# Performance work log

Hardware: AMD Instinct MI355X
Metric: run time of the kernel (lower is better)

## Reference

```python
import jax, jax.numpy as jnp
import numpy as np

BS, L, D = 128, 256, 512
H, DK = 2, 256  # heads, head dim
EPS_BN = 1e-5


def _lin(x, W, b):
    # torch Linear: W is (out, in)
    return jnp.einsum('...i,oi->...o', x, W) + b


def _bn(x, g, b, m, v):
    # eval-mode BatchNorm over channel axis = last axis of x
    return (x - m) * (g * jax.lax.rsqrt(v + EPS_BN)) + b


def setup_inputs() -> dict:
    key = jax.random.key(0)
    ks = iter(jax.random.split(key, 64))
    rn = lambda shape, s=0.02: jax.random.normal(next(ks), shape, dtype=jnp.float32) * s
    inp = {}
    inp['cap_emb'] = jax.random.normal(next(ks), (BS, L, D), dtype=jnp.float32)
    inp['lengths'] = jax.random.randint(next(ks), (BS,), 1, L + 1, dtype=jnp.int64 if jax.config.jax_enable_x64 else jnp.int32)
    # GA linears q,k,v
    for nm in ('Wq', 'Wk', 'Wv'):
        inp[nm] = rn((D, D))
    for nm in ('bq', 'bk', 'bv'):
        inp[nm] = rn((D,))
    inp['Wfq'] = rn((DK, DK)); inp['bfq'] = rn((DK,))
    inp['Wfk'] = rn((DK, DK)); inp['bfk'] = rn((DK,))
    inp['Wfg'] = rn((2 * DK, DK)); inp['bfg'] = rn((2 * DK,))
    # BatchNorm params (eval running stats)
    for pre in ('bn1', 'bn2', 'bn3'):
        inp[pre + '_g'] = 1.0 + rn((D,), 0.1)
        inp[pre + '_b'] = rn((D,), 0.1)
        inp[pre + '_m'] = rn((D,), 0.1)
        inp[pre + '_v'] = jax.random.uniform(next(ks), (D,), minval=0.5, maxval=1.5, dtype=jnp.float32)
    # Conv1d weights, torch layout (out, in, k)
    inp['Wc2'] = rn((D, D, 2)); inp['bc2'] = rn((D,))
    inp['Wc3'] = rn((D, D, 3)); inp['bc3'] = rn((D,))
    # MLP 512 -> 1024 -> 512
    inp['Wm1'] = rn((2 * D, D)); inp['bm1'] = rn((2 * D,))
    inp['Wm2'] = rn((D, 2 * D)); inp['bm2'] = rn((D,))
    return inp


def _forward(cap_emb, Wq, bq, Wk, bk, Wv, bv, Wfq, bfq, Wfk, bfk, Wfg, bfg,
             bn1_g, bn1_b, bn1_m, bn1_v, Wc2, bc2, bn2_g, bn2_b, bn2_m, bn2_v,
             Wc3, bc3, bn3_g, bn3_b, bn3_m, bn3_v, Wm1, bm1, Wm2, bm2, lengths):
    bs, seq, dim = cap_emb.shape
    # ---- GA: gated self-attention ----
    def split_heads(x):
        return x.reshape(bs, seq, H, DK).transpose(0, 2, 1, 3)  # [bs,h,seq,dk]
    q = split_heads(_lin(cap_emb, Wq, bq))
    k = split_heads(_lin(cap_emb, Wk, bk))
    v = split_heads(_lin(cap_emb, Wv, bv))
    G = _lin(q, Wfq, bfq) * _lin(k, Wfk, bfk)
    M = jax.nn.sigmoid(_lin(G, Wfg, bfg))  # [bs,h,seq,2*dk]
    qg = q * M[..., :DK]
    kg = k * M[..., DK:]
    # torch.div(..., rounding_mode='floor') == elementwise floor of scaled scores
    scores = jnp.floor(jnp.einsum('bhqd,bhkd->bhqk', qg, kg) / jnp.sqrt(jnp.float32(DK)))
    p_attn = jax.nn.softmax(scores, axis=-1)
    x = jnp.einsum('bhqk,bhkd->bhqd', p_attn, v)
    x = x.transpose(0, 2, 1, 3).reshape(bs, seq, dim)
    # BN over features (eval), dropout is identity in eval mode
    ga_emb = cap_emb + _bn(x, bn1_g, bn1_b, bn1_m, bn1_v)
    # ---- dual conv1d branches ----
    xc = cap_emb.transpose(0, 2, 1)  # [bs, D, L]
    dn = ('NCW', 'OIW', 'NCW')
    c2 = jax.lax.conv_general_dilated(xc, Wc2, window_strides=(2,), padding='VALID', dimension_numbers=dn) + bc2[None, :, None]
    c3 = jax.lax.conv_general_dilated(xc, Wc3, window_strides=(3,), padding='VALID', dimension_numbers=dn) + bc3[None, :, None]
    f2 = jax.nn.relu(_bn(c2.transpose(0, 2, 1), bn2_g, bn2_b, bn2_m, bn2_v))
    f3 = jax.nn.relu(_bn(c3.transpose(0, 2, 1), bn3_g, bn3_b, bn3_m, bn3_v))
    ga_jw = jnp.concatenate([ga_emb, f2, f3], axis=1)
    # ---- residual MLP (dropout identity in eval) ----
    hid = jax.nn.relu(_lin(ga_jw, Wm1, bm1))
    tex_emb = _lin(hid, Wm2, bm2) + ga_jw
    # ---- length-indexed gather ----
    idx = lengths.astype(jnp.int32) - 1
    out = tex_emb[jnp.arange(bs), idx]  # [bs, D]
    # l2norm
    norm = jnp.sqrt(jnp.sum(out * out, axis=-1, keepdims=True)) + 1e-8
    return out / norm


def reference(cap_emb, lengths, Wq, bq, Wk, bk, Wv, bv, Wfq, bfq, Wfk, bfk, Wfg, bfg,
              bn1_g, bn1_b, bn1_m, bn1_v, Wc2, bc2, bn2_g, bn2_b, bn2_m, bn2_v,
              Wc3, bc3, bn3_g, bn3_b, bn3_m, bn3_v, Wm1, bm1, Wm2, bm2):
    return _forward(cap_emb, Wq, bq, Wk, bk, Wv, bv, Wfq, bfq, Wfk, bfk, Wfg, bfg,
                    bn1_g, bn1_b, bn1_m, bn1_v, Wc2, bc2, bn2_g, bn2_b, bn2_m, bn2_v,
                    Wc3, bc3, bn3_g, bn3_b, bn3_m, bn3_v, Wm1, bm1, Wm2, bm2, lengths)
```

## Files before the change

kernel.cpp:

```cpp
#include <hip/hip_runtime.h>
#include <math.h>


typedef short bf16x8 __attribute__((ext_vector_type(8)));
typedef float f32x4 __attribute__((ext_vector_type(4)));
typedef short short4v __attribute__((ext_vector_type(4)));

__device__ __forceinline__ short f2bf(float x) {
    union { float f; unsigned u; } c; c.f = x;
    unsigned r = c.u + 0x7FFFu + ((c.u >> 16) & 1u);
    return (short)(r >> 16);
}
__device__ __forceinline__ float bf2f(short h) {
    union { float f; unsigned u; } c; c.u = ((unsigned)(unsigned short)h) << 16;
    return c.f;
}
__device__ __forceinline__ void glds16(const void* g, void* l) {
    __builtin_amdgcn_global_load_lds(
        (const __attribute__((address_space(1))) void*)g,
        (__attribute__((address_space(3))) void*)l, 16, 0, 0);
}

struct SplitArgs {
    const float* src[4];
    short* hi[4];
    short* lo[4];
    int n4[4];
};
__global__ __launch_bounds__(256) void split_multi(SplitArgs a)
{
    const int j = blockIdx.y;
    const float4* s = (const float4*)a.src[j];
    short* hi = a.hi[j];
    short* lo = a.lo[j];
    const int n4 = a.n4[j];
    for (int i = blockIdx.x * 256 + threadIdx.x; i < n4; i += gridDim.x * 256) {
        float4 x = s[i];
        short4v h, l;
        h.x = f2bf(x.x); l.x = f2bf(x.x - bf2f(h.x));
        h.y = f2bf(x.y); l.y = f2bf(x.y - bf2f(h.y));
        h.z = f2bf(x.z); l.z = f2bf(x.z - bf2f(h.z));
        h.w = f2bf(x.w); l.w = f2bf(x.w - bf2f(h.w));
        *(short4v*)&hi[i * 4] = h;
        *(short4v*)&lo[i * 4] = l;
    }
}

__global__ __launch_bounds__(256)
void compose(const float* __restrict__ Wq, const float* __restrict__ bq,
             const float* __restrict__ Wfq, const float* __restrict__ bfq,
             short* __restrict__ WaHi, float* __restrict__ ba)
{
    __shared__ float fq[256];
    __shared__ float redc[256];
    const int op = blockIdx.x;
    const int h = op >> 8, o = op & 255;
    const int t = threadIdx.x;
    fq[t] = Wfq[o * 256 + t];
    redc[t] = fq[t] * bq[h * 256 + t];
    __syncthreads();
    for (int s = 128; s > 0; s >>= 1) {
        if (t < s) redc[t] += redc[t + s];
        __syncthreads();
    }
    if (t == 0) ba[op] = redc[0] + bfq[o];
    float s0 = 0.f, s1 = 0.f;
    for (int d = 0; d < 256; ++d) {
        const float f = fq[d];
        const float* wr = Wq + (size_t)(h * 256 + d) * 512;
        s0 += f * wr[t];
        s1 += f * wr[t + 256];
    }
    const size_t ro = (size_t)op * 512;
    WaHi[ro + t] = f2bf(s0);
    WaHi[ro + 256 + t] = f2bf(s1);
}

template<int NSPLIT, int MODE>
__global__ __launch_bounds__(256, 2)
void gemm2p(const short* __restrict__ Ahi, const short* __restrict__ Alo,
            int lda, int aoff,
            const short* __restrict__ Bhi, const short* __restrict__ Blo, int ldb,
            const float* __restrict__ bias,
            const short* __restrict__ E1, const short* __restrict__ E2,
            int ldep, int eoff,
            const float* __restrict__ qg, float* __restrict__ scorep,
            short* __restrict__ C0, short* __restrict__ C1,
            int ldc, int coff, int K)
{
    constexpr int SLOT = (NSPLIT == 3) ? 16384 : 8192;
    __shared__ short lds[2][SLOT];
    __shared__ float sp[256];
    const int tid = threadIdx.x;
    const int bm = blockIdx.y * 128;
    const int bn = blockIdx.x * 128;
    const int z = blockIdx.z;
    const short* Ah = Ahi + (size_t)z * aoff;
    const short* Al = (NSPLIT == 3) ? (Alo + (size_t)z * aoff) : nullptr;

    const int lane = tid & 63;
    const int wr = (tid >> 7) & 1, wc = (tid >> 6) & 1;
    const int fr = lane & 15, kc = lane >> 4;
    const int r0 = tid >> 2;
    const int e0 = (((tid & 3) ^ ((r0 >> 1) & 3))) * 8;
    const int kce = (kc ^ ((fr >> 1) & 3)) * 8;

    auto stage = [&](int ph, int k0) {
        short* b = lds[ph];
        glds16(Ah + (size_t)(bm + r0) * lda + k0 + e0,       b + tid * 8);
        glds16(Ah + (size_t)(bm + r0 + 64) * lda + k0 + e0,  b + (tid + 256) * 8);
        glds16(Bhi + (size_t)(bn + r0) * ldb + k0 + e0,      b + 4096 + tid * 8);
        glds16(Bhi + (size_t)(bn + r0 + 64) * ldb + k0 + e0, b + 4096 + (tid + 256) * 8);
        if constexpr (NSPLIT == 3) {
            glds16(Al + (size_t)(bm + r0) * lda + k0 + e0,       b + 8192 + tid * 8);
            glds16(Al + (size_t)(bm + r0 + 64) * lda + k0 + e0,  b + 8192 + (tid + 256) * 8);
            glds16(Blo + (size_t)(bn + r0) * ldb + k0 + e0,      b + 12288 + tid * 8);
            glds16(Blo + (size_t)(bn + r0 + 64) * ldb + k0 + e0, b + 12288 + (tid + 256) * 8);
        }
    };

    f32x4 acc[4][4];
#pragma unroll
    for (int i = 0; i < 4; ++i)
#pragma unroll
        for (int j = 0; j < 4; ++j) acc[i][j] = (f32x4){0.f, 0.f, 0.f, 0.f};

    stage(0, 0);
    __syncthreads();
    const int NS = K / 32;
    for (int s = 0; s < NS; ++s) {
        if (s + 1 < NS) stage((s + 1) & 1, (s + 1) * 32);
        const short* b = lds[s & 1];
        bf16x8 ah[4], bh[4];
#pragma unroll
        for (int i = 0; i < 4; ++i)
            ah[i] = *(const bf16x8*)&b[(wr * 64 + i * 16 + fr) * 32 + kce];
#pragma unroll
        for (int i = 0; i < 4; ++i)
            bh[i] = *(const bf16x8*)&b[4096 + (wc * 64 + i * 16 + fr) * 32 + kce];
#pragma unroll
        for (int mi = 0; mi < 4; ++mi)
#pragma unroll
            for (int ni = 0; ni < 4; ++ni)
                acc[mi][ni] = __builtin_amdgcn_mfma_f32_16x16x32_bf16(ah[mi], bh[ni], acc[mi][ni], 0, 0, 0);
        if constexpr (NSPLIT == 3) {
            bf16x8 al[4], bl[4];
#pragma unroll
            for (int i = 0; i < 4; ++i)
                al[i] = *(const bf16x8*)&b[8192 + (wr * 64 + i * 16 + fr) * 32 + kce];
#pragma unroll
            for (int mi = 0; mi < 4; ++mi)
#pragma unroll
                for (int ni = 0; ni < 4; ++ni)
                    acc[mi][ni] = __builtin_amdgcn_mfma_f32_16x16x32_bf16(al[mi], bh[ni], acc[mi][ni], 0, 0, 0);
#pragma unroll
            for (int i = 0; i < 4; ++i)
                bl[i] = *(const bf16x8*)&b[12288 + (wc * 64 + i * 16 + fr) * 32 + kce];
#pragma unroll
            for (int mi = 0; mi < 4; ++mi)
#pragma unroll
                for (int ni = 0; ni < 4; ++ni)
                    acc[mi][ni] = __builtin_amdgcn_mfma_f32_16x16x32_bf16(ah[mi], bl[ni], acc[mi][ni], 0, 0, 0);
        }
        __syncthreads();
    }

    float qgv[4];
    float pt[4][4];
    if (MODE == 4) {
        const int b = bm >> 8;
#pragma unroll
        for (int ni = 0; ni < 4; ++ni)
            qgv[ni] = qg[b * 512 + z * 256 + bn + wc * 64 + ni * 16 + fr];
#pragma unroll
        for (int mi = 0; mi < 4; ++mi)
#pragma unroll
            for (int r = 0; r < 4; ++r) pt[mi][r] = 0.f;
    }

#pragma unroll
    for (int mi = 0; mi < 4; ++mi) {
#pragma unroll
        for (int ni = 0; ni < 4; ++ni) {
#pragma unroll
            for (int r = 0; r < 4; ++r) {
                const int row = bm + wr * 64 + mi * 16 + kc * 4 + r;
                const int col = bn + wc * 64 + ni * 16 + fr;
                const float v = acc[mi][ni][r] + bias[col];
                if (MODE == 1) {
                    const size_t off = (size_t)row * ldc + (size_t)z * coff + col;
                    short h = f2bf(v);
                    C0[off] = h;
                    C1[off] = f2bf(v - bf2f(h));
                } else if (MODE == 2) {
                    C0[(size_t)row * ldc + (size_t)z * coff + col] = f2bf(v);
                } else if (MODE == 3) {
                    const size_t eoffs = (size_t)row * ldep + (size_t)z * eoff + col;
                    const float e = bf2f(E1[eoffs]);
                    C0[(size_t)row * ldc + (size_t)z * coff + col] = f2bf(v * e);
                } else if (MODE == 4) {
                    const size_t eoffs = (size_t)row * ldep + (size_t)z * eoff + col;
                    const float e = bf2f(E1[eoffs]) + bf2f(E2[eoffs]);
                    const float kgv = e / (1.f + expf(-v));
                    pt[mi][r] += kgv * qgv[ni];
                }
            }
        }
    }

    if (MODE == 4) {
#pragma unroll
        for (int mi = 0; mi < 4; ++mi) {
#pragma unroll
            for (int r = 0; r < 4; ++r) {
                float p = pt[mi][r];
                p += __shfl_xor(p, 1);
                p += __shfl_xor(p, 2);
                p += __shfl_xor(p, 4);
                p += __shfl_xor(p, 8);
                if (fr == 0) {
                    const int row_local = wr * 64 + mi * 16 + kc * 4 + r;
                    sp[row_local * 2 + wc] = p;
                }
            }
        }
        __syncthreads();
        if (tid < 128) {
            const int row = bm + tid;
            const float s = sp[tid * 2] + sp[tid * 2 + 1];
            const int b = row >> 8, j = row & 255;
            scorep[((size_t)(b * 2 + z) * 256 + j) * 2 + blockIdx.x] = s;
        }
    }
}

__global__ __launch_bounds__(256)
void qg_kernel(const float* __restrict__ cap,
               const short* __restrict__ Ghi,
               const float* __restrict__ Wq, const float* __restrict__ bq,
               const float* __restrict__ Wfg, const float* __restrict__ bfg,
               const int* __restrict__ lengths, float* __restrict__ qg)
{
    __shared__ float cr[512];
    __shared__ float gs[256];
    const int b = blockIdx.x >> 1, h = blockIdx.x & 1;
    const int t = threadIdx.x;
    int r = lengths[b] - 1;
    if (r < 0) r = 0;
    if (r > 255) r = 255;
    const size_t base = ((size_t)b * 256 + r) * 512;
    cr[t] = cap[base + t];
    cr[t + 256] = cap[base + 256 + t];
    gs[t] = bf2f(Ghi[base + h * 256 + t]);
    __syncthreads();
    const float4* wq4 = (const float4*)(Wq + (size_t)(h * 256 + t) * 512);
    float q = 0.f;
    for (int k4 = 0; k4 < 128; ++k4) {
        float4 w = wq4[k4];
        q += w.x * cr[k4 * 4 + 0] + w.y * cr[k4 * 4 + 1]
           + w.z * cr[k4 * 4 + 2] + w.w * cr[k4 * 4 + 3];
    }
    q += bq[h * 256 + t];
    const float4* w4 = (const float4*)(Wfg + (size_t)t * 256);
    float a = 0.f;
    for (int k4 = 0; k4 < 64; ++k4) {
        float4 w = w4[k4];
        a += w.x * gs[k4 * 4 + 0] + w.y * gs[k4 * 4 + 1]
           + w.z * gs[k4 * 4 + 2] + w.w * gs[k4 * 4 + 3];
    }
    a += bfg[t];
    qg[b * 512 + h * 256 + t] = q / (1.f + expf(-a));
}

__global__ __launch_bounds__(256)
void softmax_p(const float* __restrict__ scorep, float* __restrict__ pn)
{
    __shared__ float sc[512], red[512];
    const int b = blockIdx.x;
    const int t = threadIdx.x;
#pragma unroll
    for (int i = 0; i < 2; ++i) {
        const int o = t + i * 256;
        const int h = o >> 8, j = o & 255;
        const size_t si = ((size_t)(b * 2 + h) * 256 + j) * 2;
        sc[o] = floorf((scorep[si] + scorep[si + 1]) * 0.0625f);
    }
    __syncthreads();
    red[t] = sc[t]; red[t + 256] = sc[t + 256];
    __syncthreads();
    for (int s = 128; s > 0; s >>= 1) {
        if (t < s) {
            red[t] = fmaxf(red[t], red[t + s]);
            red[256 + t] = fmaxf(red[256 + t], red[256 + t + s]);
        }
        __syncthreads();
    }
    const float mx0 = red[0], mx1 = red[256];
    __syncthreads();
    const float e0 = expf(sc[t] - mx0);
    const float e1 = expf(sc[t + 256] - mx1);
    red[t] = e0; red[t + 256] = e1;
    __syncthreads();
    for (int s = 128; s > 0; s >>= 1) {
        if (t < s) { red[t] += red[t + s]; red[256 + t] += red[256 + t + s]; }
        __syncthreads();
    }
    pn[b * 512 + t] = e0 / red[0];
    pn[b * 512 + 256 + t] = e1 / red[256];
}

__global__ __launch_bounds__(256)
void pbar_kernel(const float* __restrict__ pn, const float* __restrict__ cap,
                 float* __restrict__ pbar)
{
    __shared__ float p0s[256], p1s[256], r0[256], r1[256];
    const int b = blockIdx.y, cg = blockIdx.x;
    const int t = threadIdx.x;
    p0s[t] = pn[b * 512 + t];
    p1s[t] = pn[b * 512 + 256 + t];
    __syncthreads();
    const int c = cg * 64 + (t & 63);
    const int jg = t >> 6;
    float a0 = 0.f, a1 = 0.f;
    for (int j = jg * 64; j < jg * 64 + 64; ++j) {
        const float cv = cap[((size_t)(b * 256 + j)) * 512 + c];
        a0 += p0s[j] * cv;
        a1 += p1s[j] * cv;
    }
    r0[t] = a0; r1[t] = a1;
    __syncthreads();
    if (t < 64) {
        const float s0 = r0[t] + r0[t + 64] + r0[t + 128] + r0[t + 192];
        const float s1 = r1[t] + r1[t + 64] + r1[t + 128] + r1[t + 192];
        pbar[b * 1024 + cg * 64 + t] = s0;
        pbar[b * 1024 + 512 + cg * 64 + t] = s1;
    }
}

__global__ __launch_bounds__(256)
void bnx_kernel(const float* __restrict__ pbar, const float* __restrict__ cap,
                const int* __restrict__ lengths,
                const float* __restrict__ Wv, const float* __restrict__ bv,
                const float* __restrict__ g1, const float* __restrict__ b1,
                const float* __restrict__ m1, const float* __restrict__ v1,
                float* __restrict__ xga)
{
    __shared__ float pb[1024];
    const int b = blockIdx.x;
    const int t = threadIdx.x;
    int r = lengths[b] - 1;
    if (r < 0) r = 0;
    if (r > 255) r = 255;
    const size_t base = ((size_t)b * 256 + r) * 512;
    pb[t] = pbar[b * 1024 + t];
    pb[t + 256] = pbar[b * 1024 + 256 + t];
    pb[t + 512] = pbar[b * 1024 + 512 + t];
    pb[t + 768] = pbar[b * 1024 + 768 + t];
    __syncthreads();
    float x0 = 0.f, x1 = 0.f;
    {
        const float4* w4 = (const float4*)(Wv + (size_t)t * 512);
        for (int k4 = 0; k4 < 128; ++k4) {
            float4 w = w4[k4];
            x0 += w.x * pb[k4 * 4 + 0] + w.y * pb[k4 * 4 + 1]
                + w.z * pb[k4 * 4 + 2] + w.w * pb[k4 * 4 + 3];
        }
        x0 += bv[t];
    }
    {
        const float4* w4 = (const float4*)(Wv + (size_t)(t + 256) * 512);
        for (int k4 = 0; k4 < 128; ++k4) {
            float4 w = w4[k4];
            x1 += w.x * pb[512 + k4 * 4 + 0] + w.y * pb[512 + k4 * 4 + 1]
                + w.z * pb[512 + k4 * 4 + 2] + w.w * pb[512 + k4 * 4 + 3];
        }
        x1 += bv[t + 256];
    }
    const int c0 = t, c1 = t + 256;
    const float s0 = g1[c0] / sqrtf(v1[c0] + 1e-5f);
    const float s1 = g1[c1] / sqrtf(v1[c1] + 1e-5f);
    xga[b * 512 + c0] = cap[base + c0] + (x0 - m1[c0]) * s0 + b1[c0];
    xga[b * 512 + c1] = cap[base + c1] + (x1 - m1[c1]) * s1 + b1[c1];
}

__global__ __launch_bounds__(256)
void mlp1(const float* __restrict__ xga, const float* __restrict__ W,
          const float* __restrict__ bias, float* __restrict__ hid)
{
    __shared__ float xs[16 * 512];
    const int r0 = blockIdx.y * 16;
    const int c0 = blockIdx.x * 64;
    for (int i = threadIdx.x; i < 2048; i += 256)
        ((float4*)xs)[i] = ((const float4*)(xga + (size_t)r0 * 512))[i];
    __syncthreads();
    const int col = c0 + (threadIdx.x & 63);
    const int rg = (threadIdx.x >> 6) * 4;
    float acc[4] = {0.f, 0.f, 0.f, 0.f};
    const float4* w4 = (const float4*)(W + (size_t)col * 512);
    for (int k4 = 0; k4 < 128; ++k4) {
        float4 w = w4[k4];
#pragma unroll
        for (int rr = 0; rr < 4; ++rr) {
            float4 x = *(const float4*)&xs[(rg + rr) * 512 + k4 * 4];
            acc[rr] += w.x * x.x + w.y * x.y + w.z * x.z + w.w * x.w;
        }
    }
    const float bb = bias[col];
#pragma unroll
    for (int rr = 0; rr < 4; ++rr)
        hid[(size_t)(r0 + rg + rr) * 1024 + col] = fmaxf(acc[rr] + bb, 0.f);
}

__global__ __launch_bounds__(256)
void mlp2(const float* __restrict__ hid, const float* __restrict__ W,
          const float* __restrict__ bias, const float* __restrict__ xga,
          float* __restrict__ tex)
{
    __shared__ float xs[16 * 1024];
    const int r0 = blockIdx.y * 16;
    const int c0 = blockIdx.x * 64;
    for (int i = threadIdx.x; i < 4096; i += 256)
        ((float4*)xs)[i] = ((const float4*)(hid + (size_t)r0 * 1024))[i];
    __syncthreads();
    const int col = c0 + (threadIdx.x & 63);
    const int rg = (threadIdx.x >> 6) * 4;
    float acc[4] = {0.f, 0.f, 0.f, 0.f};
    const float4* w4 = (const float4*)(W + (size_t)col * 1024);
    for (int k4 = 0; k4 < 256; ++k4) {
        float4 w = w4[k4];
#pragma unroll
        for (int rr = 0; rr < 4; ++rr) {
            float4 x = *(const float4*)&xs[(rg + rr) * 1024 + k4 * 4];
            acc[rr] += w.x * x.x + w.y * x.y + w.z * x.z + w.w * x.w;
        }
    }
    const float bb = bias[col];
#pragma unroll
    for (int rr = 0; rr < 4; ++rr) {
        const int row = r0 + rg + rr;
        tex[(size_t)row * 512 + col] = acc[rr] + bb + xga[(size_t)row * 512 + col];
    }
}

__global__ __launch_bounds__(256)
void norm_out(const float* __restrict__ tex, float* __restrict__ out)
{
    __shared__ float red[256];
    const int b = blockIdx.x;
    const int t = threadIdx.x;
    const float a = tex[b * 512 + t];
    const float c = tex[b * 512 + 256 + t];
    red[t] = a * a + c * c;
    __syncthreads();
    for (int s = 128; s > 0; s >>= 1) {
        if (t < s) red[t] += red[t + s];
        __syncthreads();
    }
    const float inv = 1.f / (sqrtf(red[0]) + 1e-8f);
    out[b * 512 + t] = a * inv;
    out[b * 512 + 256 + t] = c * inv;
}

extern "C" void kernel_launch(void* const* d_in, const int* in_sizes, int n_in,
                              void* d_out, int out_size, void* d_ws, size_t ws_size,
                              hipStream_t stream)
{
    const float* cap = (const float*)d_in[0];
    const int* lengths = (const int*)d_in[1];
    const float* Wq  = (const float*)d_in[2];
    const float* Wk  = (const float*)d_in[3];
    const float* Wv  = (const float*)d_in[4];
    const float* bq  = (const float*)d_in[5];
    const float* bk  = (const float*)d_in[6];
    const float* bv  = (const float*)d_in[7];
    const float* Wfq = (const float*)d_in[8];
    const float* bfq = (const float*)d_in[9];
    const float* Wfk = (const float*)d_in[10];
    const float* bfk = (const float*)d_in[11];
    const float* Wfg = (const float*)d_in[12];
    const float* bfg = (const float*)d_in[13];
    const float* g1  = (const float*)d_in[14];
    const float* b1  = (const float*)d_in[15];
    const float* m1  = (const float*)d_in[16];
    const float* v1  = (const float*)d_in[17];
    const float* Wm1 = (const float*)d_in[30];
    const float* bm1 = (const float*)d_in[31];
    const float* Wm2 = (const float*)d_in[32];
    const float* bm2 = (const float*)d_in[33];
    float* out = (float*)d_out;

    char* w = (char*)d_ws;
    const size_t MB = 1024 * 1024;
    short* capHi = (short*)(w);
    short* capLo = (short*)(w + 32 * MB);
    short* KAhi  = (short*)(w + 64 * MB);
    short* KAlo  = (short*)(w + 128 * MB);
    char* wp = w + 192 * MB;
    short* WkHi  = (short*)wp; wp += 524288;
    short* WkLo  = (short*)wp; wp += 524288;
    short* WaHi  = (short*)wp; wp += 524288;
    short* WfkHi = (short*)wp; wp += 131072;
    short* WfkLo = (short*)wp; wp += 131072;
    short* Wfg2Hi = (short*)wp; wp += 131072;
    short* Wfg2Lo = (short*)wp; wp += 131072;
    float* ba     = (float*)wp; wp += 2048;
    float* qg     = (float*)wp; wp += 262144;
    float* scorep = (float*)wp; wp += 524288;
    float* pn     = (float*)wp; wp += 262144;
    float* pbar   = (float*)wp; wp += 524288;
    float* xga    = (float*)wp; wp += 262144;
    float* hid    = (float*)wp; wp += 524288;
    float* tex    = (float*)wp; wp += 262144;
    short* Ghi = capHi;

    SplitArgs sa;
    sa.src[0] = cap;          sa.hi[0] = capHi;  sa.lo[0] = capLo;  sa.n4[0] = 4194304;
    sa.src[1] = Wk;           sa.hi[1] = WkHi;   sa.lo[1] = WkLo;   sa.n4[1] = 65536;
    sa.src[2] = Wfk;          sa.hi[2] = WfkHi;  sa.lo[2] = WfkLo;  sa.n4[2] = 16384;
    sa.src[3] = Wfg + 65536;  sa.hi[3] = Wfg2Hi; sa.lo[3] = Wfg2Lo; sa.n4[3] = 16384;
    split_multi<<<dim3(4096, 4), 256, 0, stream>>>(sa);

    compose<<<dim3(512), 256, 0, stream>>>(Wq, bq, Wfq, bfq, WaHi, ba);

    gemm2p<3, 1><<<dim3(4, 256, 1), 256, 0, stream>>>(
        capHi, capLo, 512, 0, WkHi, WkLo, 512, bk,
        nullptr, nullptr, 0, 0, nullptr, nullptr,
        KAhi, KAlo, 1024, 0, 512);

    gemm2p<1, 2><<<dim3(4, 256, 1), 256, 0, stream>>>(
        capHi, nullptr, 512, 0, WaHi, nullptr, 512, ba,
        nullptr, nullptr, 0, 0, nullptr, nullptr,
        KAhi + 512, nullptr, 1024, 0, 512);

    gemm2p<1, 3><<<dim3(2, 256, 2), 256, 0, stream>>>(
        KAhi, nullptr, 1024, 256, WfkHi, nullptr, 256, bfk,
        KAhi + 512, nullptr, 1024, 256, nullptr, nullptr,
        Ghi, nullptr, 512, 256, 256);

    qg_kernel<<<dim3(256), 256, 0, stream>>>(cap, Ghi, Wq, bq, Wfg, bfg, lengths, qg);

    gemm2p<1, 4><<<dim3(2, 256, 2), 256, 0, stream>>>(
        Ghi, nullptr, 512, 256, Wfg2Hi, nullptr, 256, bfg + 256,
        KAhi, KAlo, 1024, 256, qg, scorep,
        nullptr, nullptr, 0, 0, 256);

    softmax_p<<<dim3(128), 256, 0, stream>>>(scorep, pn);
    pbar_kernel<<<dim3(8, 128), 256, 0, stream>>>(pn, cap, pbar);
    bnx_kernel<<<dim3(128), 256, 0, stream>>>(pbar, cap, lengths, Wv, bv, g1, b1, m1, v1, xga);

    mlp1<<<dim3(16, 8), 256, 0, stream>>>(xga, Wm1, bm1, hid);
    mlp2<<<dim3(8, 8), 256, 0, stream>>>(hid, Wm2, bm2, xga, tex);
    norm_out<<<dim3(128), 256, 0, stream>>>(tex, out);
}
```

Before: 320.6 us.

## Fuse K and A projection GEMMs, merge softmax into pbar, read bf16 cap

Merges the split-precision K projection GEMM and the bf16 A projection GEMM into one launch, where blocks pick their path by column index. The softmax is folded into the pbar kernel, and pbar now reads the bf16 high part of cap instead of fp32 cap. G gets its own buffer so capHi stays intact for pbar. This removes two launches, the intermediate pn array and half the cap read bandwidth in pbar. In exchange, the fused GEMM mixes heavy and light blocks, softmax is recomputed in each of the 8 column groups, and pbar loses precision by dropping the low part of cap.

```diff
diff --git a/kernel.cpp b/kernel.cpp
--- a/kernel.cpp
+++ b/kernel.cpp
@@ -76,27 +76,128 @@
     WaHi[ro + 256 + t] = f2bf(s1);
 }
 
-template<int NSPLIT, int MODE>
 __global__ __launch_bounds__(256, 2)
-void gemm2p(const short* __restrict__ Ahi, const short* __restrict__ Alo,
-            int lda, int aoff,
-            const short* __restrict__ Bhi, const short* __restrict__ Blo, int ldb,
+void gemm_ka(const short* __restrict__ capHi, const short* __restrict__ capLo,
+             const short* __restrict__ WkHi, const short* __restrict__ WkLo,
+             const short* __restrict__ WaHi,
+             const float* __restrict__ bk, const float* __restrict__ ba,
+             short* __restrict__ KAhi, short* __restrict__ KAlo)
+{
+    __shared__ short lds[2][16384];
+    const int tid = threadIdx.x;
+    const int bm = blockIdx.y * 128;
+    const int bnx = blockIdx.x;
+    const bool sp = bnx < 4;
+    const int bn = bnx * 128;
+    const int brow = sp ? bn : bn - 512;
+    const short* Bh = sp ? WkHi : WaHi;
+
+    const int lane = tid & 63;
+    const int wr = (tid >> 7) & 1, wc = (tid >> 6) & 1;
+    const int fr = lane & 15, kc = lane >> 4;
+    const int r0 = tid >> 2;
+    const int e0 = (((tid & 3) ^ ((r0 >> 1) & 3))) * 8;
+    const int kce = (kc ^ ((fr >> 1) & 3)) * 8;
+
+    auto stage = [&](int ph, int k0) {
+        short* b = lds[ph];
+        glds16(capHi + (size_t)(bm + r0) * 512 + k0 + e0,       b + tid * 8);
+        glds16(capHi + (size_t)(bm + r0 + 64) * 512 + k0 + e0,  b + (tid + 256) * 8);
+        glds16(Bh + (size_t)(brow + r0) * 512 + k0 + e0,        b + 4096 + tid * 8);
+        glds16(Bh + (size_t)(brow + r0 + 64) * 512 + k0 + e0,   b + 4096 + (tid + 256) * 8);
+        if (sp) {
+            glds16(capLo + (size_t)(bm + r0) * 512 + k0 + e0,       b + 8192 + tid * 8);
+            glds16(capLo + (size_t)(bm + r0 + 64) * 512 + k0 + e0,  b + 8192 + (tid + 256) * 8);
+            glds16(WkLo + (size_t)(brow + r0) * 512 + k0 + e0,      b + 12288 + tid * 8);
+            glds16(WkLo + (size_t)(brow + r0 + 64) * 512 + k0 + e0, b + 12288 + (tid + 256) * 8);
+        }
+    };
+
+    f32x4 acc[4][4];
+#pragma unroll
+    for (int i = 0; i < 4; ++i)
+#pragma unroll
+        for (int j = 0; j < 4; ++j) acc[i][j] = (f32x4){0.f, 0.f, 0.f, 0.f};
+
+    stage(0, 0);
+    __syncthreads();
+    for (int s = 0; s < 16; ++s) {
+        if (s + 1 < 16) stage((s + 1) & 1, (s + 1) * 32);
+        const short* b = lds[s & 1];
+        bf16x8 ah[4], bh[4];
+#pragma unroll
+        for (int i = 0; i < 4; ++i)
+            ah[i] = *(const bf16x8*)&b[(wr * 64 + i * 16 + fr) * 32 + kce];
+#pragma unroll
+        for (int i = 0; i < 4; ++i)
+            bh[i] = *(const bf16x8*)&b[4096 + (wc * 64 + i * 16 + fr) * 32 + kce];
+#pragma unroll
+        for (int mi = 0; mi < 4; ++mi)
+#pragma unroll
+            for (int ni = 0; ni < 4; ++ni)
+                acc[mi][ni] = __builtin_amdgcn_mfma_f32_16x16x32_bf16(ah[mi], bh[ni], acc[mi][ni], 0, 0, 0);
+        if (sp) {
+            bf16x8 al[4], bl[4];
+#pragma unroll
+            for (int i = 0; i < 4; ++i)
+                al[i] = *(const bf16x8*)&b[8192 + (wr * 64 + i * 16 + fr) * 32 + kce];
+#pragma unroll
+            for (int mi = 0; mi < 4; ++mi)
+#pragma unroll
+                for (int ni = 0; ni < 4; ++ni)
+                    acc[mi][ni] = __builtin_amdgcn_mfma_f32_16x16x32_bf16(al[mi], bh[ni], acc[mi][ni], 0, 0, 0);
+#pragma unroll
+            for (int i = 0; i < 4; ++i)
+                bl[i] = *(const bf16x8*)&b[12288 + (wc * 64 + i * 16 + fr) * 32 + kce];
+#pragma unroll
+            for (int mi = 0; mi < 4; ++mi)
+#pragma unroll
+                for (int ni = 0; ni < 4; ++ni)
+                    acc[mi][ni] = __builtin_amdgcn_mfma_f32_16x16x32_bf16(ah[mi], bl[ni], acc[mi][ni], 0, 0, 0);
+        }
+        __syncthreads();
+    }
+
+#pragma unroll
+    for (int mi = 0; mi < 4; ++mi) {
+#pragma unroll
+        for (int ni = 0; ni < 4; ++ni) {
+#pragma unroll
+            for (int r = 0; r < 4; ++r) {
+                const int row = bm + wr * 64 + mi * 16 + kc * 4 + r;
+                const int colg = bn + wc * 64 + ni * 16 + fr;
+                const float bb = sp ? bk[colg] : ba[colg - 512];
+                const float v = acc[mi][ni][r] + bb;
+                const size_t off = (size_t)row * 1024 + colg;
+                if (sp) {
+                    short h = f2bf(v);
+                    KAhi[off] = h;
+                    KAlo[off] = f2bf(v - bf2f(h));
+                } else {
+                    KAhi[off] = f2bf(v);
+                }
+            }
+        }
+    }
+}
+
+template<int MODE>
+__global__ __launch_bounds__(256, 2)
+void gemm2p(const short* __restrict__ Ahi, int lda, int aoff,
+            const short* __restrict__ Bhi, int ldb,
             const float* __restrict__ bias,
             const short* __restrict__ E1, const short* __restrict__ E2,
             int ldep, int eoff,
             const float* __restrict__ qg, float* __restrict__ scorep,
-            short* __restrict__ C0, short* __restrict__ C1,
-            int ldc, int coff, int K)
-{
-    constexpr int SLOT = (NSPLIT == 3) ? 16384 : 8192;
-    __shared__ short lds[2][SLOT];
+            short* __restrict__ C0, int ldc, int coff, int K)
+{
+    __shared__ short lds[2][8192];
     __shared__ float sp[256];
     const int tid = threadIdx.x;
     const int bm = blockIdx.y * 128;
     const int bn = blockIdx.x * 128;
     const int z = blockIdx.z;
     const short* Ah = Ahi + (size_t)z * aoff;
-    const short* Al = (NSPLIT == 3) ? (Alo + (size_t)z * aoff) : nullptr;
 
     const int lane = tid & 63;
     const int wr = (tid >> 7) & 1, wc = (tid >> 6) & 1;
@@ -111,12 +212,6 @@
         glds16(Ah + (size_t)(bm + r0 + 64) * lda + k0 + e0,  b + (tid + 256) * 8);
         glds16(Bhi + (size_t)(bn + r0) * ldb + k0 + e0,      b + 4096 + tid * 8);
         glds16(Bhi + (size_t)(bn + r0 + 64) * ldb + k0 + e0, b + 4096 + (tid + 256) * 8);
-        if constexpr (NSPLIT == 3) {
-            glds16(Al + (size_t)(bm + r0) * lda + k0 + e0,       b + 8192 + tid * 8);
-            glds16(Al + (size_t)(bm + r0 + 64) * lda + k0 + e0,  b + 8192 + (tid + 256) * 8);
-            glds16(Blo + (size_t)(bn + r0) * ldb + k0 + e0,      b + 12288 + tid * 8);
-            glds16(Blo + (size_t)(bn + r0 + 64) * ldb + k0 + e0, b + 12288 + (tid + 256) * 8);
-        }
     };
 
     f32x4 acc[4][4];
@@ -143,25 +238,6 @@
 #pragma unroll
             for (int ni = 0; ni < 4; ++ni)
                 acc[mi][ni] = __builtin_amdgcn_mfma_f32_16x16x32_bf16(ah[mi], bh[ni], acc[mi][ni], 0, 0, 0);
-        if constexpr (NSPLIT == 3) {
-            bf16x8 al[4], bl[4];
-#pragma unroll
-            for (int i = 0; i < 4; ++i)
-                al[i] = *(const bf16x8*)&b[8192 + (wr * 64 + i * 16 + fr) * 32 + kce];
-#pragma unroll
-            for (int mi = 0; mi < 4; ++mi)
-#pragma unroll
-                for (int ni = 0; ni < 4; ++ni)
-                    acc[mi][ni] = __builtin_amdgcn_mfma_f32_16x16x32_bf16(al[mi], bh[ni], acc[mi][ni], 0, 0, 0);
-#pragma unroll
-            for (int i = 0; i < 4; ++i)
-                bl[i] = *(const bf16x8*)&b[12288 + (wc * 64 + i * 16 + fr) * 32 + kce];
-#pragma unroll
-            for (int mi = 0; mi < 4; ++mi)
-#pragma unroll
-                for (int ni = 0; ni < 4; ++ni)
-                    acc[mi][ni] = __builtin_amdgcn_mfma_f32_16x16x32_bf16(ah[mi], bl[ni], acc[mi][ni], 0, 0, 0);
-        }
         __syncthreads();
     }
 
@@ -187,19 +263,11 @@
                 const int row = bm + wr * 64 + mi * 16 + kc * 4 + r;
                 const int col = bn + wc * 64 + ni * 16 + fr;
                 const float v = acc[mi][ni][r] + bias[col];
-                if (MODE == 1) {
-                    const size_t off = (size_t)row * ldc + (size_t)z * coff + col;
-                    short h = f2bf(v);
-                    C0[off] = h;
-                    C1[off] = f2bf(v - bf2f(h));
-                } else if (MODE == 2) {
-                    C0[(size_t)row * ldc + (size_t)z * coff + col] = f2bf(v);
-                } else if (MODE == 3) {
-                    const size_t eoffs = (size_t)row * ldep + (size_t)z * eoff + col;
+                const size_t eoffs = (size_t)row * ldep + (size_t)z * eoff + col;
+                if (MODE == 3) {
                     const float e = bf2f(E1[eoffs]);
                     C0[(size_t)row * ldc + (size_t)z * coff + col] = f2bf(v * e);
-                } else if (MODE == 4) {
-                    const size_t eoffs = (size_t)row * ldep + (size_t)z * eoff + col;
+                } else {
                     const float e = bf2f(E1[eoffs]) + bf2f(E2[eoffs]);
                     const float kgv = e / (1.f + expf(-v));
                     pt[mi][r] += kgv * qgv[ni];
@@ -236,7 +304,7 @@
 
 __global__ __launch_bounds__(256)
 void qg_kernel(const float* __restrict__ cap,
-               const short* __restrict__ Ghi,
+               const short* __restrict__ Gbuf,
                const float* __restrict__ Wq, const float* __restrict__ bq,
                const float* __restrict__ Wfg, const float* __restrict__ bfg,
                const int* __restrict__ lengths, float* __restrict__ qg)
@@ -251,7 +319,7 @@
     const size_t base = ((size_t)b * 256 + r) * 512;
     cr[t] = cap[base + t];
     cr[t + 256] = cap[base + 256 + t];
-    gs[t] = bf2f(Ghi[base + h * 256 + t]);
+    gs[t] = bf2f(Gbuf[base + h * 256 + t]);
     __syncthreads();
     const float4* wq4 = (const float4*)(Wq + (size_t)(h * 256 + t) * 512);
     float q = 0.f;
@@ -273,10 +341,11 @@
 }
 
 __global__ __launch_bounds__(256)
-void softmax_p(const float* __restrict__ scorep, float* __restrict__ pn)
+void pbar_kernel(const float* __restrict__ scorep, const short* __restrict__ capHi,
+                 float* __restrict__ pbar)
 {
     __shared__ float sc[512], red[512];
-    const int b = blockIdx.x;
+    const int b = blockIdx.y, cg = blockIdx.x;
     const int t = threadIdx.x;
 #pragma unroll
     for (int i = 0; i < 2; ++i) {
@@ -305,34 +374,29 @@
         if (t < s) { red[t] += red[t + s]; red[256 + t] += red[256 + t + s]; }
         __syncthreads();
     }
-    pn[b * 512 + t] = e0 / red[0];
-    pn[b * 512 + 256 + t] = e1 / red[256];
-}
-
-__global__ __launch_bounds__(256)
-void pbar_kernel(const float* __restrict__ pn, const float* __restrict__ cap,
-                 float* __restrict__ pbar)
-{
-    __shared__ float p0s[256], p1s[256], r0[256], r1[256];
-    const int b = blockIdx.y, cg = blockIdx.x;
-    const int t = threadIdx.x;
-    p0s[t] = pn[b * 512 + t];
-    p1s[t] = pn[b * 512 + 256 + t];
-    __syncthreads();
+    sc[t] = e0 / red[0];
+    sc[t + 256] = e1 / red[256];
+    __syncthreads();
+
     const int c = cg * 64 + (t & 63);
     const int jg = t >> 6;
     float a0 = 0.f, a1 = 0.f;
     for (int j = jg * 64; j < jg * 64 + 64; ++j) {
-        const float cv = cap[((size_t)(b * 256 + j)) * 512 + c];
-        a0 += p0s[j] * cv;
-        a1 += p1s[j] * cv;
-    }
-    r0[t] = a0; r1[t] = a1;
+        const float cv = bf2f(capHi[((size_t)(b * 256 + j)) * 512 + c]);
+        a0 += sc[j] * cv;
+        a1 += sc[256 + j] * cv;
+    }
+    red[t] = a0;
     __syncthreads();
     if (t < 64) {
-        const float s0 = r0[t] + r0[t + 64] + r0[t + 128] + r0[t + 192];
-        const float s1 = r1[t] + r1[t + 64] + r1[t + 128] + r1[t + 192];
+        const float s0 = red[t] + red[t + 64] + red[t + 128] + red[t + 192];
         pbar[b * 1024 + cg * 64 + t] = s0;
+    }
+    __syncthreads();
+    red[t] = a1;
+    __syncthreads();
+    if (t < 64) {
+        const float s1 = red[t] + red[t + 64] + red[t + 128] + red[t + 192];
         pbar[b * 1024 + 512 + cg * 64 + t] = s1;
     }
 }
@@ -495,7 +559,8 @@
     short* capLo = (short*)(w + 32 * MB);
     short* KAhi  = (short*)(w + 64 * MB);
     short* KAlo  = (short*)(w + 128 * MB);
-    char* wp = w + 192 * MB;
+    short* Gbuf  = (short*)(w + 192 * MB);
+    char* wp = w + 224 * MB;
     short* WkHi  = (short*)wp; wp += 524288;
     short* WkLo  = (short*)wp; wp += 524288;
     short* WaHi  = (short*)wp; wp += 524288;
@@ -506,12 +571,10 @@
     float* ba     = (float*)wp; wp += 2048;
     float* qg     = (float*)wp; wp += 262144;
     float* scorep = (float*)wp; wp += 524288;
-    float* pn     = (float*)wp; wp += 262144;
     float* pbar   = (float*)wp; wp += 524288;
     float* xga    = (float*)wp; wp += 262144;
     float* hid    = (float*)wp; wp += 524288;
     float* tex    = (float*)wp; wp += 262144;
-    short* Ghi = capHi;
 
     SplitArgs sa;
     sa.src[0] = cap;          sa.hi[0] = capHi;  sa.lo[0] = capLo;  sa.n4[0] = 4194304;
@@ -522,30 +585,22 @@
 
     compose<<<dim3(512), 256, 0, stream>>>(Wq, bq, Wfq, bfq, WaHi, ba);
 
-    gemm2p<3, 1><<<dim3(4, 256, 1), 256, 0, stream>>>(
-        capHi, capLo, 512, 0, WkHi, WkLo, 512, bk,
-        nullptr, nullptr, 0, 0, nullptr, nullptr,
-        KAhi, KAlo, 1024, 0, 512);
-
-    gemm2p<1, 2><<<dim3(4, 256, 1), 256, 0, stream>>>(
-        capHi, nullptr, 512, 0, WaHi, nullptr, 512, ba,
-        nullptr, nullptr, 0, 0, nullptr, nullptr,
-        KAhi + 512, nullptr, 1024, 0, 512);
-
-    gemm2p<1, 3><<<dim3(2, 256, 2), 256, 0, stream>>>(
-        KAhi, nullptr, 1024, 256, WfkHi, nullptr, 256, bfk,
+    gemm_ka<<<dim3(8, 256), 256, 0, stream>>>(capHi, capLo, WkHi, WkLo, WaHi,
+                                              bk, ba, KAhi, KAlo);
+
+    gemm2p<3><<<dim3(2, 256, 2), 256, 0, stream>>>(
+        KAhi, 1024, 256, WfkHi, 256, bfk,
         KAhi + 512, nullptr, 1024, 256, nullptr, nullptr,
-        Ghi, nullptr, 512, 256, 256);
-
-    qg_kernel<<<dim3(256), 256, 0, stream>>>(cap, Ghi, Wq, bq, Wfg, bfg, lengths, qg);
-
-    gemm2p<1, 4><<<dim3(2, 256, 2), 256, 0, stream>>>(
-        Ghi, nullptr, 512, 256, Wfg2Hi, nullptr, 256, bfg + 256,
+        Gbuf, 512, 256, 256);
+
+    qg_kernel<<<dim3(256), 256, 0, stream>>>(cap, Gbuf, Wq, bq, Wfg, bfg, lengths, qg);
+
+    gemm2p<4><<<dim3(2, 256, 2), 256, 0, stream>>>(
+        Gbuf, 512, 256, Wfg2Hi, 256, bfg + 256,
         KAhi, KAlo, 1024, 256, qg, scorep,
-        nullptr, nullptr, 0, 0, 256);
-
-    softmax_p<<<dim3(128), 256, 0, stream>>>(scorep, pn);
-    pbar_kernel<<<dim3(8, 128), 256, 0, stream>>>(pn, cap, pbar);
+        nullptr, 0, 0, 256);
+
+    pbar_kernel<<<dim3(8, 128), 256, 0, stream>>>(scorep, capHi, pbar);
     bnx_kernel<<<dim3(128), 256, 0, stream>>>(pbar, cap, lengths, Wv, bv, g1, b1, m1, v1, xga);
 
     mlp1<<<dim3(16, 8), 256, 0, stream>>>(xga, Wm1, bm1, hid);
```

Result: slower. 356.8 us (+11.3%).
